# Performance work log

Measured on AMD Instinct MI355X. Metric: run time of the kernel, lower is better.

Reference implementation:

```python
import jax, jax.numpy as jnp
import numpy as np

BETA = 0.25  # commitment-loss weight from init_kwargs

B, T, D, K = 16, 2048, 256, 1024


def setup_inputs() -> dict:
    key = jax.random.key(0)
    k1, k2 = jax.random.split(key)
    z_e = jax.random.normal(k1, (B, T, D), dtype=jnp.float32)
    codebook = jax.random.normal(k2, (K, D), dtype=jnp.float32)
    return {"z_e": z_e, "codebook": codebook}


def reference(z_e, codebook):
    # dot_z_embedding: tensordot over channel dim -> (B, T, K)
    dot = jnp.einsum("btd,kd->btk", z_e, codebook)
    norm_sq_z = jnp.sum(jnp.square(z_e), axis=-1, keepdims=True)      # (B, T, 1)
    norm_sq_e = jnp.sum(jnp.square(codebook), axis=-1)                # (K,)
    dist = -2.0 * dot + norm_sq_z + norm_sq_e                         # (B, T, K)
    ids = jnp.argmin(dist, axis=-1)                                   # (B, T) int
    z_q = codebook[ids]                                               # (B, T, D)
    # losses: tf.norm over the quantised axis, then mean
    loss_commit = jnp.mean(jnp.linalg.norm(jax.lax.stop_gradient(z_e) - z_q, axis=-1))
    loss_codebook = jnp.mean(jnp.linalg.norm(z_e - jax.lax.stop_gradient(z_q), axis=-1))
    loss_vq = loss_codebook + BETA * loss_commit
    similarity = dot / jnp.sqrt(norm_sq_z) / jnp.sqrt(norm_sq_e)      # (B, T, K) cosine
    return z_q, similarity, ids, loss_vq
```

## Files before the change

### kernel.cpp

```cpp
#include <hip/hip_runtime.h>


#define M_ROWS 32768
#define KCODES 1024
#define DDIM   256
#define ENC_BIG 33554432.0f

typedef __bf16 bf16_t;
typedef __attribute__((ext_vector_type(8))) bf16_t bf16x8;
typedef __attribute__((ext_vector_type(4))) float f32x4;

__device__ __forceinline__ unsigned short f2bf(float f) {
  unsigned u = __float_as_uint(f);
  u += 0x7FFFu + ((u >> 16) & 1u);
  return (unsigned short)(u >> 16);
}

__device__ __forceinline__ float wave_sum(float p) {
#pragma unroll
  for (int o = 1; o < 64; o <<= 1) p += __shfl_xor(p, o);
  return p;
}
__device__ __forceinline__ float wave_min(float p) {
#pragma unroll
  for (int o = 1; o < 64; o <<= 1) p = fminf(p, __shfl_xor(p, o));
  return p;
}

__global__ __launch_bounds__(256) void prep_cb_kernel(
    const float* __restrict__ cb, unsigned short* __restrict__ cbb,
    float* __restrict__ nse, float* __restrict__ rsqe)
{
  const int t = threadIdx.x;
  const int lane = t & 63;
  const int r = blockIdx.x * 4 + (t >> 6);
  const float4 e = ((const float4*)cb)[(size_t)r * 64 + lane];
  ushort4 u;
  u.x = f2bf(e.x); u.y = f2bf(e.y); u.z = f2bf(e.z); u.w = f2bf(e.w);
  ((ushort4*)cbb)[(size_t)r * 64 + lane] = u;
  float p = wave_sum(e.x*e.x + e.y*e.y + e.z*e.z + e.w*e.w);
  if (lane == 0) { nse[r] = p; rsqe[r] = 1.0f / sqrtf(p); }
}

__global__ __launch_bounds__(256, 2) void fused_kernel(
    const float* __restrict__ ze, const float* __restrict__ cb,
    const unsigned short* __restrict__ cbb,
    const float* __restrict__ nse_g, const float* __restrict__ rsqe_g,
    float* __restrict__ sim, float* __restrict__ zq, float* __restrict__ ids,
    float* __restrict__ partials)
{
  __shared__ __attribute__((aligned(128))) unsigned short A[64 * 256];
  __shared__ __attribute__((aligned(128))) unsigned short Bt[128 * 64];
  __shared__ float s_nse[KCODES];
  __shared__ float s_rsqe[KCODES];
  __shared__ float s_rsqz[64];
  __shared__ float cand_lds[64 * 32];
  __shared__ float s_part[4];

  const int t = threadIdx.x;
  const int wv = t >> 6, lane = t & 63;
  const int r16 = lane & 15, g = lane >> 4;
  const int wm = wv >> 1, wn = wv & 1;
  const long row0 = (long)blockIdx.x * 64;

  ((float4*)s_nse)[t]  = ((const float4*)nse_g)[t];
  ((float4*)s_rsqe)[t] = ((const float4*)rsqe_g)[t];

#pragma unroll
  for (int k = 0; k < 16; ++k) {
    const int row = wv + 4 * k;
    const float4 z = ((const float4*)ze)[(row0 + row) * 64 + lane];
    const float p = wave_sum(z.x*z.x + z.y*z.y + z.z*z.z + z.w*z.w);
    if (lane == 0) s_rsqz[row] = 1.0f / sqrtf(p);
    ushort4 u;
    u.x = f2bf(z.x); u.y = f2bf(z.y); u.z = f2bf(z.z); u.w = f2bf(z.w);
    const int q  = lane >> 1;
    const int ph = (q & 24) | ((q ^ (row & 7)) & 7);
    *(ushort4*)((char*)A + row * 512 + ph * 16 + (lane & 1) * 8) = u;
  }
  __syncthreads();

  f32x4 acc[2][4] = {};
  const int rr = lane >> 3, qq = lane & 7;
  const int sq = ((qq ^ rr) << 3);

  for (int kt = 0; kt < 32; ++kt) {
    const int c = kt >> 2, kk = kt & 3;
    const int col0 = c * 128, k0 = kk * 64;
#pragma unroll
    for (int i = 0; i < 4; ++i) {
      const int rbase = wv * 32 + i * 8;
      const unsigned short* src = cbb + ((size_t)(col0 + rbase + rr)) * DDIM + k0 + sq;
      __builtin_amdgcn_global_load_lds((const __attribute__((address_space(1))) void*)src,
                                       (__attribute__((address_space(3))) void*)&Bt[rbase * 64],
                                       16, 0, 0);
    }
    __syncthreads();
#pragma unroll
    for (int ks = 0; ks < 2; ++ks) {
      bf16x8 af[2], bf[4];
#pragma unroll
      for (int mi = 0; mi < 2; ++mi) {
        const int r = wm * 32 + mi * 16 + r16;
        const int ql = kk * 8 + ks * 4 + g;
        const int ph = (ql & 24) | ((ql ^ (r & 7)) & 7);
        af[mi] = *(const bf16x8*)((const char*)A + r * 512 + ph * 16);
      }
#pragma unroll
      for (int ni = 0; ni < 4; ++ni) {
        const int r = wn * 64 + ni * 16 + r16;
        const int ph = (ks * 4 + g) ^ (r & 7);
        bf[ni] = *(const bf16x8*)((const char*)Bt + r * 128 + ph * 16);
      }
#pragma unroll
      for (int mi = 0; mi < 2; ++mi)
#pragma unroll
        for (int ni = 0; ni < 4; ++ni)
          acc[mi][ni] = __builtin_amdgcn_mfma_f32_16x16x32_bf16(af[mi], bf[ni], acc[mi][ni], 0, 0, 0);
    }
    __syncthreads();

    if (kk == 3) {
      const int strip = c * 2 + wn;
#pragma unroll
      for (int mi = 0; mi < 2; ++mi) {
#pragma unroll
        for (int j = 0; j < 4; ++j) {
          const int rloc = wm * 32 + mi * 16 + g * 4 + j;
          const long row = row0 + rloc;
          const float rz = s_rsqz[rloc];
          float* so = sim + (size_t)row * KCODES + col0 + wn * 64 + r16;
          float e1 = ENC_BIG, e2 = ENC_BIG;
#pragma unroll
          for (int ni = 0; ni < 4; ++ni) {
            const int colk = col0 + wn * 64 + ni * 16 + r16;
            const float d = acc[mi][ni][j];
            so[ni * 16] = d * rz * s_rsqe[colk];
            const float v = s_nse[colk] - 2.0f * d;
            const float enc = floorf((v + 1024.0f) * 8.0f) * 1024.0f + (float)colk;
            if (enc < e1) { e2 = e1; e1 = enc; } else e2 = fminf(e2, enc);
          }
#pragma unroll
          for (int m = 1; m < 16; m <<= 1) {
            const float p1 = __shfl_xor(e1, m);
            const float p2 = __shfl_xor(e2, m);
            const float n1 = fminf(e1, p1);
            const float n2 = fminf(fmaxf(e1, p1), fminf(e2, p2));
            e1 = n1; e2 = n2;
          }
          if (r16 == 0) {
            cand_lds[rloc * 32 + strip * 2]     = e1;
            cand_lds[rloc * 32 + strip * 2 + 1] = e2;
          }
        }
      }
#pragma unroll
      for (int mi = 0; mi < 2; ++mi)
#pragma unroll
        for (int ni = 0; ni < 4; ++ni)
          acc[mi][ni] = (f32x4)(0.0f);
    }
  }
  __syncthreads();

  float loss_local = 0.0f;
  float4 zr = ((const float4*)ze)[(row0 + wv * 16) * 64 + lane];
  for (int i = 0; i < 16; ++i) {
    const int rloc = wv * 16 + i;
    const long row = row0 + rloc;
    const float4 zc = zr;
    if (i < 15) zr = ((const float4*)ze)[(row + 1) * 64 + lane];

    const float e = (lane < 32) ? cand_lds[rloc * 32 + lane] : ENC_BIG;
    const float m_enc = wave_min(e);
    const float qmin  = floorf(m_enc * 0.0009765625f);
    const float ql    = floorf(e * 0.0009765625f);
    unsigned long long msk = __ballot(ql <= qmin + 16.0f);
    int kbest;
    if (__popcll(msk) == 1) {
      kbest = ((int)m_enc) & 1023;
    } else {
      float tbest = INFINITY; kbest = KCODES;
      while (msk) {
        const int lb = __ffsll(msk) - 1;
        msk &= msk - 1;
        const int kc = ((int)__shfl(e, lb)) & 1023;
        const float4 er = ((const float4*)cb)[(size_t)kc * 64 + lane];
        const float p = wave_sum(zc.x*er.x + zc.y*er.y + zc.z*er.z + zc.w*er.w);
        const float tv = s_nse[kc] - 2.0f * p;
        if (tv < tbest || (tv == tbest && kc < kbest)) { tbest = tv; kbest = kc; }
      }
    }

    const float4 er = ((const float4*)cb)[(size_t)kbest * 64 + lane];
    ((float4*)zq)[(size_t)row * 64 + lane] = er;
    const float dx = zc.x - er.x, dy = zc.y - er.y, dz = zc.z - er.z, dw = zc.w - er.w;
    const float ss = wave_sum(dx*dx + dy*dy + dz*dz + dw*dw);
    if (lane == 0) {
      ids[row] = (float)kbest;
      loss_local += sqrtf(ss);
    }
  }
  if (lane == 0) s_part[wv] = loss_local;
  __syncthreads();
  if (t == 0)
    partials[blockIdx.x] = (s_part[0] + s_part[1]) + (s_part[2] + s_part[3]);
}

__global__ __launch_bounds__(256) void finalize_kernel(
    const float* __restrict__ partials, float* __restrict__ out_loss)
{
  __shared__ float s[4];
  const int t = threadIdx.x;
  float p = partials[t] + partials[t + 256];
  p = wave_sum(p);
  if ((t & 63) == 0) s[t >> 6] = p;
  __syncthreads();
  if (t == 0) out_loss[0] = 1.25f * ((s[0] + s[1]) + (s[2] + s[3])) / 32768.0f;
}

extern "C" void kernel_launch(void* const* d_in, const int* in_sizes, int n_in,
                              void* d_out, int out_size, void* d_ws, size_t ws_size,
                              hipStream_t stream) {
  const float* ze = (const float*)d_in[0];
  const float* cb = (const float*)d_in[1];

  float* out  = (float*)d_out;
  float* zq   = out;
  float* sim  = out + 8388608;
  float* ids  = out + 41943040;
  float* lout = out + 41975808;

  char* w = (char*)d_ws;
  unsigned short* cbb = (unsigned short*)w;
  float* nse      = (float*)(w + 524288);
  float* rsqe     = (float*)(w + 528384);
  float* partials = (float*)(w + 532480);

  prep_cb_kernel<<<256, 256, 0, stream>>>(cb, cbb, nse, rsqe);
  fused_kernel<<<512, 256, 0, stream>>>(ze, cb, cbb, nse, rsqe, sim, zq, ids, partials);
  finalize_kernel<<<1, 256, 0, stream>>>(partials, lout);
}
```

Measured before the change: 86.32 us.

## Split fused VQ kernel into 2D-tiled GEMM, select, and zq/loss kernels

Replaces the single fused kernel, which looped over all codebook columns for a 64-row tile, with a 128x128 tiled GEMM kernel over a 2D grid of 2048 blocks. A block-index swizzle groups blocks for L2 reuse, and the fp32-to-bf16 conversion of z_e is fused into the k-loop. Per-strip argmin candidates go to a scratch region aliased onto the zq output. Separate select and zq/loss kernels then pick the final code and write zq and the loss partials. This raises parallelism and MFMA tile efficiency, at the cost of extra launches, each block re-reading and re-converting z_e for every column tile, and a global round-trip for the candidates.

```diff
diff --git a/kernel.cpp b/kernel.cpp
--- a/kernel.cpp
+++ b/kernel.cpp
@@ -10,10 +10,10 @@
 typedef __attribute__((ext_vector_type(8))) bf16_t bf16x8;
 typedef __attribute__((ext_vector_type(4))) float f32x4;
 
-__device__ __forceinline__ unsigned short f2bf(float f) {
+__device__ __forceinline__ unsigned f2bf(float f) {
   unsigned u = __float_as_uint(f);
   u += 0x7FFFu + ((u >> 16) & 1u);
-  return (unsigned short)(u >> 16);
+  return u >> 16;
 }
 
 __device__ __forceinline__ float wave_sum(float p) {
@@ -36,57 +36,38 @@
   const int r = blockIdx.x * 4 + (t >> 6);
   const float4 e = ((const float4*)cb)[(size_t)r * 64 + lane];
   ushort4 u;
-  u.x = f2bf(e.x); u.y = f2bf(e.y); u.z = f2bf(e.z); u.w = f2bf(e.w);
+  u.x = (unsigned short)f2bf(e.x); u.y = (unsigned short)f2bf(e.y);
+  u.z = (unsigned short)f2bf(e.z); u.w = (unsigned short)f2bf(e.w);
   ((ushort4*)cbb)[(size_t)r * 64 + lane] = u;
   float p = wave_sum(e.x*e.x + e.y*e.y + e.z*e.z + e.w*e.w);
   if (lane == 0) { nse[r] = p; rsqe[r] = 1.0f / sqrtf(p); }
 }
 
-__global__ __launch_bounds__(256, 2) void fused_kernel(
-    const float* __restrict__ ze, const float* __restrict__ cb,
-    const unsigned short* __restrict__ cbb,
-    const float* __restrict__ nse_g, const float* __restrict__ rsqe_g,
-    float* __restrict__ sim, float* __restrict__ zq, float* __restrict__ ids,
-    float* __restrict__ partials)
-{
-  __shared__ __attribute__((aligned(128))) unsigned short A[64 * 256];
+__global__ __launch_bounds__(256, 2) void gemm_kernel(
+    const float* __restrict__ ze, const unsigned short* __restrict__ cbb,
+    const float* __restrict__ rsqe_g, const float* __restrict__ nse_g,
+    float* __restrict__ sim, float* __restrict__ cand)
+{
+  __shared__ __attribute__((aligned(128))) unsigned short A[128 * 64];
   __shared__ __attribute__((aligned(128))) unsigned short Bt[128 * 64];
-  __shared__ float s_nse[KCODES];
-  __shared__ float s_rsqe[KCODES];
-  __shared__ float s_rsqz[64];
-  __shared__ float cand_lds[64 * 32];
-  __shared__ float s_part[4];
+  __shared__ float s_rsqz[128];
 
   const int t = threadIdx.x;
   const int wv = t >> 6, lane = t & 63;
-  const int r16 = lane & 15, g = lane >> 4;
-  const int wm = wv >> 1, wn = wv & 1;
-  const long row0 = (long)blockIdx.x * 64;
-
-  ((float4*)s_nse)[t]  = ((const float4*)nse_g)[t];
-  ((float4*)s_rsqe)[t] = ((const float4*)rsqe_g)[t];
-
-#pragma unroll
-  for (int k = 0; k < 16; ++k) {
-    const int row = wv + 4 * k;
-    const float4 z = ((const float4*)ze)[(row0 + row) * 64 + lane];
-    const float p = wave_sum(z.x*z.x + z.y*z.y + z.z*z.z + z.w*z.w);
-    if (lane == 0) s_rsqz[row] = 1.0f / sqrtf(p);
-    ushort4 u;
-    u.x = f2bf(z.x); u.y = f2bf(z.y); u.z = f2bf(z.z); u.w = f2bf(z.w);
-    const int q  = lane >> 1;
-    const int ph = (q & 24) | ((q ^ (row & 7)) & 7);
-    *(ushort4*)((char*)A + row * 512 + ph * 16 + (lane & 1) * 8) = u;
-  }
-  __syncthreads();
-
-  f32x4 acc[2][4] = {};
+  const int bid = blockIdx.x;
+  const int swz = (bid & 7) * 256 + (bid >> 3);
+  const long row0 = (long)(swz >> 3) * 128;
+  const int  col0 = (swz & 7) * 128;
+
+  f32x4 acc[4][4] = {};
+
   const int rr = lane >> 3, qq = lane & 7;
   const int sq = ((qq ^ rr) << 3);
 
-  for (int kt = 0; kt < 32; ++kt) {
-    const int c = kt >> 2, kk = kt & 3;
-    const int col0 = c * 128, k0 = kk * 64;
+  float nrm[4] = {0.f, 0.f, 0.f, 0.f};
+
+  for (int kt = 0; kt < 4; ++kt) {
+    const int k0 = kt * 64;
 #pragma unroll
     for (int i = 0; i < 4; ++i) {
       const int rbase = wv * 32 + i * 8;
@@ -95,113 +76,142 @@
                                        (__attribute__((address_space(3))) void*)&Bt[rbase * 64],
                                        16, 0, 0);
     }
+#pragma unroll
+    for (int i = 0; i < 4; ++i) {
+      const int idx = i * 256 + t;
+      const int ar = idx >> 3, aq = idx & 7;
+      const float4* p = (const float4*)(ze + (row0 + ar) * (size_t)DDIM + k0 + aq * 8);
+      const float4 x = p[0], y = p[1];
+      nrm[i] += x.x*x.x + x.y*x.y + x.z*x.z + x.w*x.w
+              + y.x*y.x + y.y*y.y + y.z*y.z + y.w*y.w;
+      uint4 u;
+      u.x = f2bf(x.x) | (f2bf(x.y) << 16);
+      u.y = f2bf(x.z) | (f2bf(x.w) << 16);
+      u.z = f2bf(y.x) | (f2bf(y.y) << 16);
+      u.w = f2bf(y.z) | (f2bf(y.w) << 16);
+      *(uint4*)((char*)A + ar * 128 + ((aq ^ (ar & 7)) << 4)) = u;
+    }
     __syncthreads();
+
+    const int r16 = lane & 15, g = lane >> 4;
+    const int wm = wv >> 1, wn = wv & 1;
 #pragma unroll
     for (int ks = 0; ks < 2; ++ks) {
-      bf16x8 af[2], bf[4];
-#pragma unroll
-      for (int mi = 0; mi < 2; ++mi) {
-        const int r = wm * 32 + mi * 16 + r16;
-        const int ql = kk * 8 + ks * 4 + g;
-        const int ph = (ql & 24) | ((ql ^ (r & 7)) & 7);
-        af[mi] = *(const bf16x8*)((const char*)A + r * 512 + ph * 16);
+      bf16x8 af[4], bfr[4];
+#pragma unroll
+      for (int mi = 0; mi < 4; ++mi) {
+        const int r = wm * 64 + mi * 16 + r16;
+        const int ph = ((ks * 4 + g) ^ (r & 7)) << 4;
+        af[mi] = *(const bf16x8*)((const char*)A + r * 128 + ph);
       }
 #pragma unroll
       for (int ni = 0; ni < 4; ++ni) {
         const int r = wn * 64 + ni * 16 + r16;
-        const int ph = (ks * 4 + g) ^ (r & 7);
-        bf[ni] = *(const bf16x8*)((const char*)Bt + r * 128 + ph * 16);
-      }
-#pragma unroll
-      for (int mi = 0; mi < 2; ++mi)
+        const int ph = ((ks * 4 + g) ^ (r & 7)) << 4;
+        bfr[ni] = *(const bf16x8*)((const char*)Bt + r * 128 + ph);
+      }
+#pragma unroll
+      for (int mi = 0; mi < 4; ++mi)
 #pragma unroll
         for (int ni = 0; ni < 4; ++ni)
-          acc[mi][ni] = __builtin_amdgcn_mfma_f32_16x16x32_bf16(af[mi], bf[ni], acc[mi][ni], 0, 0, 0);
+          acc[mi][ni] = __builtin_amdgcn_mfma_f32_16x16x32_bf16(af[mi], bfr[ni], acc[mi][ni], 0, 0, 0);
     }
     __syncthreads();
-
-    if (kk == 3) {
-      const int strip = c * 2 + wn;
-#pragma unroll
-      for (int mi = 0; mi < 2; ++mi) {
-#pragma unroll
-        for (int j = 0; j < 4; ++j) {
-          const int rloc = wm * 32 + mi * 16 + g * 4 + j;
-          const long row = row0 + rloc;
-          const float rz = s_rsqz[rloc];
-          float* so = sim + (size_t)row * KCODES + col0 + wn * 64 + r16;
-          float e1 = ENC_BIG, e2 = ENC_BIG;
-#pragma unroll
-          for (int ni = 0; ni < 4; ++ni) {
-            const int colk = col0 + wn * 64 + ni * 16 + r16;
-            const float d = acc[mi][ni][j];
-            so[ni * 16] = d * rz * s_rsqe[colk];
-            const float v = s_nse[colk] - 2.0f * d;
-            const float enc = floorf((v + 1024.0f) * 8.0f) * 1024.0f + (float)colk;
-            if (enc < e1) { e2 = e1; e1 = enc; } else e2 = fminf(e2, enc);
-          }
-#pragma unroll
-          for (int m = 1; m < 16; m <<= 1) {
-            const float p1 = __shfl_xor(e1, m);
-            const float p2 = __shfl_xor(e2, m);
-            const float n1 = fminf(e1, p1);
-            const float n2 = fminf(fmaxf(e1, p1), fminf(e2, p2));
-            e1 = n1; e2 = n2;
-          }
-          if (r16 == 0) {
-            cand_lds[rloc * 32 + strip * 2]     = e1;
-            cand_lds[rloc * 32 + strip * 2 + 1] = e2;
-          }
-        }
-      }
-#pragma unroll
-      for (int mi = 0; mi < 2; ++mi)
-#pragma unroll
-        for (int ni = 0; ni < 4; ++ni)
-          acc[mi][ni] = (f32x4)(0.0f);
-    }
+  }
+
+#pragma unroll
+  for (int i = 0; i < 4; ++i) {
+    float p = nrm[i];
+    p += __shfl_xor(p, 1); p += __shfl_xor(p, 2); p += __shfl_xor(p, 4);
+    if ((t & 7) == 0) s_rsqz[(i * 256 + t) >> 3] = 1.0f / sqrtf(p);
   }
   __syncthreads();
 
-  float loss_local = 0.0f;
-  float4 zr = ((const float4*)ze)[(row0 + wv * 16) * 64 + lane];
-  for (int i = 0; i < 16; ++i) {
-    const int rloc = wv * 16 + i;
-    const long row = row0 + rloc;
-    const float4 zc = zr;
-    if (i < 15) zr = ((const float4*)ze)[(row + 1) * 64 + lane];
-
-    const float e = (lane < 32) ? cand_lds[rloc * 32 + lane] : ENC_BIG;
-    const float m_enc = wave_min(e);
-    const float qmin  = floorf(m_enc * 0.0009765625f);
-    const float ql    = floorf(e * 0.0009765625f);
-    unsigned long long msk = __ballot(ql <= qmin + 16.0f);
-    int kbest;
-    if (__popcll(msk) == 1) {
-      kbest = ((int)m_enc) & 1023;
-    } else {
-      float tbest = INFINITY; kbest = KCODES;
-      while (msk) {
-        const int lb = __ffsll(msk) - 1;
-        msk &= msk - 1;
-        const int kc = ((int)__shfl(e, lb)) & 1023;
-        const float4 er = ((const float4*)cb)[(size_t)kc * 64 + lane];
-        const float p = wave_sum(zc.x*er.x + zc.y*er.y + zc.z*er.z + zc.w*er.w);
-        const float tv = s_nse[kc] - 2.0f * p;
-        if (tv < tbest || (tv == tbest && kc < kbest)) { tbest = tv; kbest = kc; }
-      }
-    }
-
-    const float4 er = ((const float4*)cb)[(size_t)kbest * 64 + lane];
-    ((float4*)zq)[(size_t)row * 64 + lane] = er;
-    const float dx = zc.x - er.x, dy = zc.y - er.y, dz = zc.z - er.z, dw = zc.w - er.w;
-    const float ss = wave_sum(dx*dx + dy*dy + dz*dz + dw*dw);
-    if (lane == 0) {
-      ids[row] = (float)kbest;
-      loss_local += sqrtf(ss);
-    }
-  }
-  if (lane == 0) s_part[wv] = loss_local;
+  const int r16 = lane & 15, g = lane >> 4;
+  const int wm = wv >> 1, wn = wv & 1;
+  const int strip = (col0 >> 6) | wn;
+#pragma unroll
+  for (int mi = 0; mi < 4; ++mi) {
+#pragma unroll
+    for (int j = 0; j < 4; ++j) {
+      const int rloc = wm * 64 + mi * 16 + g * 4 + j;
+      const long row = row0 + rloc;
+      const float rz = s_rsqz[rloc];
+      float* so = sim + (size_t)row * KCODES + col0 + wn * 64 + r16;
+      float e1 = ENC_BIG, e2 = ENC_BIG;
+#pragma unroll
+      for (int ni = 0; ni < 4; ++ni) {
+        const int colk = col0 + wn * 64 + ni * 16 + r16;
+        const float d = acc[mi][ni][j];
+        so[ni * 16] = d * rz * rsqe_g[colk];
+        const float v = nse_g[colk] - 2.0f * d;
+        const float enc = floorf((v + 1024.0f) * 8.0f) * 1024.0f + (float)colk;
+        if (enc < e1) { e2 = e1; e1 = enc; } else e2 = fminf(e2, enc);
+      }
+#pragma unroll
+      for (int m = 1; m < 16; m <<= 1) {
+        const float p1 = __shfl_xor(e1, m);
+        const float p2 = __shfl_xor(e2, m);
+        const float n1 = fminf(e1, p1);
+        const float n2 = fminf(fmaxf(e1, p1), fminf(e2, p2));
+        e1 = n1; e2 = n2;
+      }
+      if (r16 == 0)
+        ((float2*)cand)[row * 16 + strip] = make_float2(e1, e2);
+    }
+  }
+}
+
+__global__ __launch_bounds__(256) void select1_kernel(
+    const float* __restrict__ ze, const float* __restrict__ cb,
+    const float* __restrict__ cand, const float* __restrict__ nse,
+    float* __restrict__ ids)
+{
+  const int t = threadIdx.x;
+  const int lane = t & 63;
+  const int row  = blockIdx.x * 4 + (t >> 6);
+
+  const float e = (lane < 32) ? cand[(size_t)row * 32 + lane] : ENC_BIG;
+  const float m_enc = wave_min(e);
+  const float qmin  = floorf(m_enc * 0.0009765625f);
+  const float ql    = floorf(e * 0.0009765625f);
+  unsigned long long msk = __ballot(ql <= qmin + 16.0f);
+  int kbest;
+  if (__popcll(msk) == 1) {
+    kbest = ((int)m_enc) & 1023;
+  } else {
+    const float4 zr = ((const float4*)ze)[(size_t)row * 64 + lane];
+    float tbest = INFINITY; kbest = KCODES;
+    while (msk) {
+      const int lb = __ffsll(msk) - 1;
+      msk &= msk - 1;
+      const int kc = ((int)__shfl(e, lb)) & 1023;
+      const float4 er = ((const float4*)cb)[(size_t)kc * 64 + lane];
+      const float p = wave_sum(zr.x*er.x + zr.y*er.y + zr.z*er.z + zr.w*er.w);
+      const float tv = nse[kc] - 2.0f * p;
+      if (tv < tbest || (tv == tbest && kc < kbest)) { tbest = tv; kbest = kc; }
+    }
+  }
+  if (lane == 0) ids[row] = (float)kbest;
+}
+
+__global__ __launch_bounds__(256) void zq_loss_kernel(
+    const float* __restrict__ ze, const float* __restrict__ cb,
+    const float* __restrict__ ids,
+    float* __restrict__ zq, float* __restrict__ partials)
+{
+  __shared__ float s_part[4];
+  const int t = threadIdx.x;
+  const int wv = t >> 6, lane = t & 63;
+  const int row = blockIdx.x * 4 + wv;
+
+  const int kbest = (int)ids[row];
+  const float4 er = ((const float4*)cb)[(size_t)kbest * 64 + lane];
+  const float4 zr = ((const float4*)ze)[(size_t)row * 64 + lane];
+  ((float4*)zq)[(size_t)row * 64 + lane] = er;
+  const float dx = zr.x - er.x, dy = zr.y - er.y, dz = zr.z - er.z, dw = zr.w - er.w;
+  const float ss = wave_sum(dx*dx + dy*dy + dz*dz + dw*dw);
+  if (lane == 0) s_part[wv] = sqrtf(ss);
   __syncthreads();
   if (t == 0)
     partials[blockIdx.x] = (s_part[0] + s_part[1]) + (s_part[2] + s_part[3]);
@@ -212,7 +222,9 @@
 {
   __shared__ float s[4];
   const int t = threadIdx.x;
-  float p = partials[t] + partials[t + 256];
+  float p = 0.0f;
+#pragma unroll
+  for (int i = 0; i < 32; ++i) p += partials[t + i * 256];
   p = wave_sum(p);
   if ((t & 63) == 0) s[t >> 6] = p;
   __syncthreads();
@@ -231,6 +243,8 @@
   float* ids  = out + 41943040;
   float* lout = out + 41975808;
 
+  float* cand = zq;
+
   char* w = (char*)d_ws;
   unsigned short* cbb = (unsigned short*)w;
   float* nse      = (float*)(w + 524288);
@@ -238,6 +252,8 @@
   float* partials = (float*)(w + 532480);
 
   prep_cb_kernel<<<256, 256, 0, stream>>>(cb, cbb, nse, rsqe);
-  fused_kernel<<<512, 256, 0, stream>>>(ze, cb, cbb, nse, rsqe, sim, zq, ids, partials);
+  gemm_kernel<<<2048, 256, 0, stream>>>(ze, cbb, rsqe, nse, sim, cand);
+  select1_kernel<<<8192, 256, 0, stream>>>(ze, cb, cand, nse, ids);
+  zq_loss_kernel<<<8192, 256, 0, stream>>>(ze, cb, ids, zq, partials);
   finalize_kernel<<<1, 256, 0, stream>>>(partials, lout);
 }
```

Result: slower. 90.25 us (+4.6%).
